# Performance work log

Measured on AMD Instinct MI355X. Metric: run time of the kernel, lower is better.

## Reference

```python
import jax, jax.numpy as jnp
import numpy as np

B, S, E, H = 4, 1024, 256, 12  # batch, seq, emb_dim, num_heads; per-head dim == E (module quirk)


def setup_inputs() -> dict:
    key = jax.random.key(0)
    ks = jax.random.split(key, 9)
    s = 0.02
    x = jax.random.normal(ks[0], (B, S, E), dtype=jnp.float32)
    # additive causal mask (the module's tril buffer is unused; mask arrives via attention_mask)
    causal = jnp.tril(jnp.ones((S, S), dtype=jnp.float32))
    attention_mask = ((1.0 - causal) * -10000.0)[None, None, :, :]
    Wq = jax.random.normal(ks[1], (E, E * H), dtype=jnp.float32) * s
    bq = jnp.zeros((E * H,), dtype=jnp.float32)
    Wk = jax.random.normal(ks[2], (E, E * H), dtype=jnp.float32) * s
    bk = jnp.zeros((E * H,), dtype=jnp.float32)
    Wv = jax.random.normal(ks[3], (E, E * H), dtype=jnp.float32) * s
    bv = jnp.zeros((E * H,), dtype=jnp.float32)
    Wfc = jax.random.normal(ks[4], (E * H, E), dtype=jnp.float32) * s
    bfc = jnp.zeros((E,), dtype=jnp.float32)
    return {"x": x, "attention_mask": attention_mask, "Wq": Wq, "bq": bq,
            "Wk": Wk, "bk": bk, "Wv": Wv, "bv": bv, "Wfc": Wfc, "bfc": bfc}


def _split_heads(t):
    # (B, S, H*E) -> (B, H, S, E)
    b, s, _ = t.shape
    return t.reshape(b, s, H, E).transpose(0, 2, 1, 3)


def reference(x, attention_mask, Wq, bq, Wk, bk, Wv, bv, Wfc, bfc):
    q = _split_heads(x @ Wq + bq)
    k = _split_heads(x @ Wk + bk)
    v = _split_heads(x @ Wv + bv)
    scale = 1.0 / jnp.sqrt(jnp.asarray(E, dtype=x.dtype))
    scores = jnp.einsum('bhqd,bhkd->bhqk', q, k) * scale + attention_mask
    probs = jax.nn.softmax(scores, axis=-1)  # dropout p=0 in eval reference
    ctx = jnp.einsum('bhqk,bhkd->bhqd', probs, v)
    merged = ctx.transpose(0, 2, 1, 3).reshape(x.shape[0], x.shape[1], H * E)
    return merged @ Wfc + bfc
```

## Files before the change

kernel.cpp:

```cpp
#include <hip/hip_runtime.h>

#define BATCH 4
#define SEQ   1024
#define EMB   256
#define NH    12
#define EH    3072
#define MROWS 4096

typedef __attribute__((ext_vector_type(8))) short bf16x8;
typedef __attribute__((ext_vector_type(4))) float f32x4;
typedef __attribute__((ext_vector_type(4))) short short4v;

__device__ __forceinline__ short f2bf(float f) {
  union { float f; unsigned u; } x; x.f = f;
  unsigned r = x.u + 0x7fffu + ((x.u >> 16) & 1u);
  return (short)(r >> 16);
}

__device__ __forceinline__ unsigned pack_trunc(float a, float b) {
  union { float f; unsigned u; } x, y;
  x.f = a; y.f = b;
  return (x.u >> 16) | (y.u & 0xffff0000u);
}

__device__ __forceinline__ void gload_lds16(const void* g, void* l) {
  __builtin_amdgcn_global_load_lds(
      (const __attribute__((address_space(1))) unsigned*)g,
      (__attribute__((address_space(3))) unsigned*)l, 16, 0, 0);
}

__global__ __launch_bounds__(256) void cast_x_kernel(const float* __restrict__ in,
                                                     short* __restrict__ out) {
  int i = (blockIdx.x * 256 + threadIdx.x) * 4;
  float4 v = *(const float4*)(in + i);
  short4v o;
  o[0] = f2bf(v.x); o[1] = f2bf(v.y); o[2] = f2bf(v.z); o[3] = f2bf(v.w);
  *(short4v*)(out + i) = o;
}

__global__ __launch_bounds__(256) void transpose_qkv_kernel(const float* __restrict__ Wq,
                                                            const float* __restrict__ Wk,
                                                            const float* __restrict__ Wv,
                                                            short* __restrict__ Wt) {
  __shared__ float tile[32][33];
  const float* W = blockIdx.z == 0 ? Wq : (blockIdx.z == 1 ? Wk : Wv);
  short* o = Wt + (size_t)blockIdx.z * EH * EMB;
  const int n0 = blockIdx.x * 32, k0 = blockIdx.y * 32;
  const int tx = threadIdx.x & 31, ty = threadIdx.x >> 5;
#pragma unroll
  for (int i = 0; i < 4; i++)
    tile[ty + 8 * i][tx] = W[(size_t)(k0 + ty + 8 * i) * EH + n0 + tx];
  __syncthreads();
#pragma unroll
  for (int i = 0; i < 4; i++) {
    int nr = ty + 8 * i;
    o[(size_t)(n0 + nr) * EMB + k0 + tx] = f2bf(tile[tx][nr]);
  }
}

__global__ __launch_bounds__(256) void transpose_cast_kernel(const float* __restrict__ W,
                                                             short* __restrict__ Wt,
                                                             int K, int N) {
  __shared__ float tile[32][33];
  const int n0 = blockIdx.x * 32, k0 = blockIdx.y * 32;
  const int tx = threadIdx.x & 31, ty = threadIdx.x >> 5;
#pragma unroll
  for (int i = 0; i < 4; i++)
    tile[ty + 8 * i][tx] = W[(size_t)(k0 + ty + 8 * i) * N + n0 + tx];
  __syncthreads();
#pragma unroll
  for (int i = 0; i < 4; i++) {
    int nr = ty + 8 * i;
    Wt[(size_t)(n0 + nr) * K + k0 + tx] = f2bf(tile[tx][nr]);
  }
}

__global__ __launch_bounds__(256) void qkv_gemm_kernel(const short* __restrict__ A,
                                                       const short* __restrict__ Bt,
                                                       const float* __restrict__ bq,
                                                       const float* __restrict__ bk,
                                                       const float* __restrict__ bv,
                                                       short* __restrict__ qout,
                                                       short* __restrict__ kout,
                                                       short* __restrict__ vout) {
  constexpr int BM = 128, BK = 64, K = EMB;
  __shared__ short As[2][BM * BK];
  __shared__ short Bs[2][BM * BK];
  const int tid = threadIdx.x;
  const int w = tid >> 6, lane = tid & 63;
  const int wm = w >> 1, wn = w & 1;
  const int l15 = lane & 15, l4 = lane >> 4;
  const int m0 = blockIdx.x * BM, n0 = blockIdx.y * BM;

  f32x4 acc[4][4] = {};

  int srow[4], scol[4];
#pragma unroll
  for (int i = 0; i < 4; i++) {
    const int idx = i * 256 + tid;
    const int row = idx >> 3, sp = idx & 7, sl = sp ^ (row & 7);
    srow[i] = row;
    scol[i] = sl * 8;
  }

#define QKV_STAGE(bu, k0)                                                        \
  {                                                                              \
    _Pragma("unroll") for (int i = 0; i < 4; i++) {                              \
      const int idx = i * 256 + tid;                                             \
      gload_lds16(A + (size_t)(m0 + srow[i]) * K + (k0) + scol[i],               \
                  (char*)&As[bu][0] + idx * 16);                                 \
      gload_lds16(Bt + (size_t)(n0 + srow[i]) * K + (k0) + scol[i],              \
                  (char*)&Bs[bu][0] + idx * 16);                                 \
    }                                                                            \
  }

  QKV_STAGE(0, 0);
  asm volatile("s_waitcnt vmcnt(0)" ::: "memory");
  __syncthreads();

  int bu = 0;
  for (int k0 = 0; k0 < K; k0 += BK) {
    if (k0 + BK < K) QKV_STAGE(bu ^ 1, k0 + BK);

#pragma unroll
    for (int kst = 0; kst < 2; kst++) {
      const int sp = (kst * 4 + l4) ^ (l15 & 7);
      bf16x8 af[4], bfr[4];
#pragma unroll
      for (int mt = 0; mt < 4; mt++)
        af[mt] = *(const bf16x8*)&As[bu][(wm * 64 + mt * 16 + l15) * 64 + sp * 8];
#pragma unroll
      for (int nt = 0; nt < 4; nt++)
        bfr[nt] = *(const bf16x8*)&Bs[bu][(wn * 64 + nt * 16 + l15) * 64 + sp * 8];
      __builtin_amdgcn_s_setprio(1);
#pragma unroll
      for (int mt = 0; mt < 4; mt++)
#pragma unroll
        for (int nt = 0; nt < 4; nt++)
          acc[mt][nt] = __builtin_amdgcn_mfma_f32_16x16x32_bf16(af[mt], bfr[nt], acc[mt][nt], 0, 0, 0);
      __builtin_amdgcn_s_setprio(0);
    }

    asm volatile("s_waitcnt vmcnt(0)" ::: "memory");
    __syncthreads();
    bu ^= 1;
  }

  const int region = n0 / 3072;
  const float* bias = region == 0 ? bq : (region == 1 ? bk : bv);
  const float kQScale = 0.09016844f;
#pragma unroll
  for (int nt = 0; nt < 4; nt++) {
    const int n = n0 + wn * 64 + nt * 16 + l15;
    const int col = n - region * 3072;
    const float bvv = bias[col];
#pragma unroll
    for (int mt = 0; mt < 4; mt++) {
      const int mrow = m0 + wm * 64 + mt * 16 + 4 * l4;
      f32x4 v = acc[mt][nt];
      if (region == 0) {
#pragma unroll
        for (int r = 0; r < 4; r++)
          qout[(size_t)(mrow + r) * EH + col] = f2bf((v[r] + bvv) * kQScale);
      } else if (region == 1) {
#pragma unroll
        for (int r = 0; r < 4; r++)
          kout[(size_t)(mrow + r) * EH + col] = f2bf(v[r] + bvv);
      } else {
        const int bb = mrow >> 10;
        const int s  = mrow & 1023;
        const int h  = col >> 8, d = col & 255;
        short4v o4;
        o4[0] = f2bf(v[0] + bvv); o4[1] = f2bf(v[1] + bvv);
        o4[2] = f2bf(v[2] + bvv); o4[3] = f2bf(v[3] + bvv);
        *(short4v*)&vout[((size_t)(bb * NH + h) * EMB + d) * SEQ + s] = o4;
      }
    }
  }
#undef QKV_STAGE
}

__global__ __launch_bounds__(256) void fc_partial_kernel(const short* __restrict__ A,
                                                         const short* __restrict__ Bt,
                                                         float* __restrict__ Pout,
                                                         int M, int N, int K) {
  constexpr int BM = 64, BK = 128, KSL = 768;
  __shared__ short As[2][BM * BK];
  __shared__ short Bs[2][BM * BK];
  const int tid = threadIdx.x;
  const int w = tid >> 6, lane = tid & 63;
  const int wm = w >> 1, wn = w & 1;
  const int l15 = lane & 15, l4 = lane >> 4;
  const int m0 = blockIdx.x * BM, n0 = blockIdx.y * BM;
  const int kbase = blockIdx.z * KSL;
  float* P = Pout + (size_t)blockIdx.z * M * N;

  f32x4 acc[2][2] = {};

  int srow[4], scol[4];
#pragma unroll
  for (int i = 0; i < 4; i++) {
    const int idx = i * 256 + tid;
    const int row = idx >> 4, sp = idx & 15, sl = sp ^ (row & 15);
    srow[i] = row;
    scol[i] = sl * 8;
  }

#define FC_STAGE(bu, k0)                                                         \
  {                                                                              \
    _Pragma("unroll") for (int i = 0; i < 4; i++) {                              \
      const int idx = i * 256 + tid;                                             \
      gload_lds16(A + (size_t)(m0 + srow[i]) * K + (k0) + scol[i],               \
                  (char*)&As[bu][0] + idx * 16);                                 \
      gload_lds16(Bt + (size_t)(n0 + srow[i]) * K + (k0) + scol[i],              \
                  (char*)&Bs[bu][0] + idx * 16);                                 \
    }                                                                            \
  }

  FC_STAGE(0, kbase);
  asm volatile("s_waitcnt vmcnt(0)" ::: "memory");
  __syncthreads();

  int bu = 0;
  for (int k0 = kbase; k0 < kbase + KSL; k0 += BK) {
    if (k0 + BK < kbase + KSL) FC_STAGE(bu ^ 1, k0 + BK);

#pragma unroll
    for (int kst = 0; kst < 4; kst++) {
      const int sp = (kst * 4 + l4) ^ l15;
      bf16x8 af[2], bfr[2];
#pragma unroll
      for (int mt = 0; mt < 2; mt++)
        af[mt] = *(const bf16x8*)&As[bu][(wm * 32 + mt * 16 + l15) * 128 + sp * 8];
#pragma unroll
      for (int nt = 0; nt < 2; nt++)
        bfr[nt] = *(const bf16x8*)&Bs[bu][(wn * 32 + nt * 16 + l15) * 128 + sp * 8];
      __builtin_amdgcn_s_setprio(1);
#pragma unroll
      for (int mt = 0; mt < 2; mt++)
#pragma unroll
        for (int nt = 0; nt < 2; nt++)
          acc[mt][nt] = __builtin_amdgcn_mfma_f32_16x16x32_bf16(af[mt], bfr[nt], acc[mt][nt], 0, 0, 0);
      __builtin_amdgcn_s_setprio(0);
    }

    asm volatile("s_waitcnt vmcnt(0)" ::: "memory");
    __syncthreads();
    bu ^= 1;
  }

#pragma unroll
  for (int nt = 0; nt < 2; nt++) {
    const int n = n0 + wn * 32 + nt * 16 + l15;
#pragma unroll
    for (int mt = 0; mt < 2; mt++) {
      const int mrow = m0 + wm * 32 + mt * 16 + 4 * l4;
      f32x4 v = acc[mt][nt];
#pragma unroll
      for (int r = 0; r < 4; r++)
        P[(size_t)(mrow + r) * N + n] = v[r];
    }
  }
#undef FC_STAGE
}

__global__ __launch_bounds__(256) void fc_reduce_kernel(const float* __restrict__ Pin,
                                                        const float* __restrict__ bias,
                                                        float* __restrict__ out) {
  const int i4 = (blockIdx.x * 256 + threadIdx.x) * 4;
  const int n = i4 & 255;
  float4 s = *(const float4*)(bias + n);
#pragma unroll
  for (int ks = 0; ks < 4; ks++) {
    float4 p = *(const float4*)(Pin + (size_t)ks * MROWS * EMB + i4);
    s.x += p.x; s.y += p.y; s.z += p.z; s.w += p.w;
  }
  *(float4*)(out + i4) = s;
}

__global__ __launch_bounds__(512) void attn_kernel(const short* __restrict__ Q,
                                                   const short* __restrict__ Kg,
                                                   const short* __restrict__ Vt,
                                                   short* __restrict__ Ctx) {
  __shared__ short Ks[2][8192];
  __shared__ short Vs[2][8192];
  __shared__ short Ps[8][512];
  const int tid = threadIdx.x, w = tid >> 6, lane = tid & 63;
  const int l15 = lane & 15, l4 = lane >> 4;
  const int bh = blockIdx.x, b = bh / NH, h = bh % NH;
  const int slot = blockIdx.y;

  const float kMaskL2 = -14426.95f;
  const float kThrL2  = 11.5f;

  const short* Kbase = Kg + (size_t)b * SEQ * EH + h * EMB;
  const short* Vbase = Vt + (size_t)bh * EMB * SEQ;

  int koff[2], voff[2];
#pragma unroll
  for (int i = 0; i < 2; i++) {
    const int idx = i * 512 + tid;
    {
      const int kv = (idx >> 3) & 31, sp = idx & 7, sl = sp ^ (kv & 7);
      koff[i] = kv * EH + (idx >> 8) * 64 + sl * 8;
    }
    {
      const int dp = idx >> 3, sp = idx & 7, sl = sp ^ (dp & 7);
      voff[i] = (dp * 2 + (sl >> 2)) * SEQ + (sl & 3) * 8;
    }
  }

  for (int pass = 0; pass < 2; pass++) {
    const int qt = (pass == 0) ? (7 - slot) : (slot - 2);
    if (qt < 0) continue;
    const int q0 = qt * 128;
    const int qw0 = q0 + w * 16;
    const int ntiles = 4 * qt + 4;

    bf16x8 qf[8];
    {
      const short* qp = Q + (size_t)(b * SEQ + qw0 + l15) * EH + h * EMB + 8 * l4;
#pragma unroll
      for (int kst = 0; kst < 8; kst++) qf[kst] = *(const bf16x8*)(qp + 32 * kst);
    }

#pragma unroll
    for (int i = 0; i < 2; i++) {
      const int idx = i * 512 + tid;
      gload_lds16(Kbase + koff[i], (char*)&Ks[0][0] + idx * 16);
      gload_lds16(Vbase + voff[i], (char*)&Vs[0][0] + idx * 16);
    }
    asm volatile("s_waitcnt vmcnt(0)" ::: "memory");
    __syncthreads();

    f32x4 o[16] = {};
    float mst = -1e30f, lst = 0.f;

    int bu = 0;
    for (int t = 0; t < ntiles; t++) {
      const int kv0 = t * 32;

      if (t + 1 < ntiles) {
        const short* kp = Kbase + (size_t)(kv0 + 32) * EH;
        const short* vp = Vbase + kv0 + 32;
#pragma unroll
        for (int i = 0; i < 2; i++) {
          const int idx = i * 512 + tid;
          gload_lds16(kp + koff[i], (char*)&Ks[bu ^ 1][0] + idx * 16);
          gload_lds16(vp + voff[i], (char*)&Vs[bu ^ 1][0] + idx * 16);
        }
      }

      if (kv0 <= qw0 + 15) {
        f32x4 sf[2] = {};
        __builtin_amdgcn_s_setprio(1);
#pragma unroll
        for (int nt = 0; nt < 2; nt++)
#pragma unroll
          for (int kst = 0; kst < 8; kst++) {
            const int sp = (((kst & 1) << 2) + l4) ^ (l15 & 7);
            bf16x8 kf = *(const bf16x8*)&Ks[bu][(kst >> 1) * 2048 + (nt * 16 + l15) * 64 + sp * 8];
            sf[nt] = __builtin_amdgcn_mfma_f32_16x16x32_bf16(kf, qf[kst], sf[nt], 0, 0, 0);
          }
        __builtin_amdgcn_s_setprio(0);

        const bool maskt = (kv0 + 31 > qw0);
        float sval[2][4];
        float mxl = -1e30f;
#pragma unroll
        for (int nt = 0; nt < 2; nt++)
#pragma unroll
          for (int r = 0; r < 4; r++) {
            float s = sf[nt][r];
            if (maskt) {
              const int kv = kv0 + nt * 16 + 4 * l4 + r;
              s += (kv > qw0 + l15) ? kMaskL2 : 0.0f;
            }
            sval[nt][r] = s;
            mxl = fmaxf(mxl, s);
          }
        float mx = fmaxf(mxl, __shfl_xor(mxl, 16));
        mx = fmaxf(mx, __shfl_xor(mx, 32));
        const bool skipt = __all(mx <= mst + kThrL2);
        float mref, fsc;
        if (skipt) {
          fsc = 1.0f;
          mref = mst;
        } else {
          float mnew = fmaxf(mst, mx);
          fsc = exp2f(mst - mnew);
          mst = mnew;
          mref = mnew;
        }
        float pp[2][4];
        float lsum = 0.f;
#pragma unroll
        for (int nt = 0; nt < 2; nt++)
#pragma unroll
          for (int r = 0; r < 4; r++) {
            float e = exp2f(sval[nt][r] - mref);
            pp[nt][r] = e;
            lsum += e;
          }
        lst = lst * fsc + lsum;

        if (!skipt) {
          float fv[4];
#pragma unroll
          for (int r = 0; r < 4; r++)
            fv[r] = __shfl(fsc, (lane & 48) + 4 * (lane >> 4) + r);
#pragma unroll
          for (int nt = 0; nt < 16; nt++) {
            o[nt][0] *= fv[0]; o[nt][1] *= fv[1];
            o[nt][2] *= fv[2]; o[nt][3] *= fv[3];
          }
        }

#pragma unroll
        for (int nt = 0; nt < 2; nt++) {
          uint2 pk;
          pk.x = pack_trunc(pp[nt][0], pp[nt][1]);
          pk.y = pack_trunc(pp[nt][2], pp[nt][3]);
          const int col0 = nt * 16 + 4 * l4;
          const int pseg = (col0 >> 3) ^ ((l15 >> 1) & 3);
          *(uint2*)&Ps[w][l15 * 32 + pseg * 8 + (col0 & 7)] = pk;
        }

        const int aseg = l4 ^ ((l15 >> 1) & 3);
        bf16x8 af = *(const bf16x8*)&Ps[w][l15 * 32 + aseg * 8];
        const int vsp = ((l15 & 1) * 4 + l4) ^ (l15 >> 1);
        __builtin_amdgcn_s_setprio(1);
#pragma unroll
        for (int nt = 0; nt < 16; nt++) {
          const int dp = nt * 8 + (l15 >> 1);
          bf16x8 vf = *(const bf16x8*)&Vs[bu][dp * 64 + vsp * 8];
          o[nt] = __builtin_amdgcn_mfma_f32_16x16x32_bf16(af, vf, o[nt], 0, 0, 0);
        }
        __builtin_amdgcn_s_setprio(0);
      }

      asm volatile("s_waitcnt vmcnt(0)" ::: "memory");
      __syncthreads();
      bu ^= 1;
    }

    lst += __shfl_xor(lst, 16);
    lst += __shfl_xor(lst, 32);
    const float inv = 1.f / lst;
    float invv[4];
#pragma unroll
    for (int r = 0; r < 4; r++)
      invv[r] = __shfl(inv, (lane & 48) + 4 * (lane >> 4) + r);

    const int mrow = b * SEQ + qw0 + 4 * l4;
#pragma unroll
    for (int nt = 0; nt < 16; nt++) {
      const int d = h * EMB + nt * 16 + l15;
#pragma unroll
      for (int r = 0; r < 4; r++)
        Ctx[(size_t)(mrow + r) * EH + d] = f2bf(o[nt][r] * invv[r]);
    }
  }
}

extern "C" void kernel_launch(void* const* d_in, const int* in_sizes, int n_in,
                              void* d_out, int out_size, void* d_ws, size_t ws_size,
                              hipStream_t stream) {
  const float* x   = (const float*)d_in[0];
  const float* Wq  = (const float*)d_in[2];
  const float* bq  = (const float*)d_in[3];
  const float* Wk  = (const float*)d_in[4];
  const float* bk  = (const float*)d_in[5];
  const float* Wv  = (const float*)d_in[6];
  const float* bv  = (const float*)d_in[7];
  const float* Wfc = (const float*)d_in[8];
  const float* bfc = (const float*)d_in[9];
  float* out = (float*)d_out;

  short* ws    = (short*)d_ws;
  short* xb    = ws;
  short* wqkvt = xb + 1048576;
  short* wfct  = wqkvt + 3 * 786432;
  short* q     = wfct + 786432;
  short* k     = q + 12582912;
  short* vt    = k + 12582912;
  short* ctx   = vt + 12582912;
  float* fcp   = (float*)q;

  cast_x_kernel<<<1024, 256, 0, stream>>>(x, xb);
  transpose_qkv_kernel<<<dim3(EH / 32, EMB / 32, 3), 256, 0, stream>>>(Wq, Wk, Wv, wqkvt);
  transpose_cast_kernel<<<dim3(EMB / 32, EH / 32), 256, 0, stream>>>(Wfc, wfct, EH, EMB);

  qkv_gemm_kernel<<<dim3(MROWS / 128, 9216 / 128), 256, 0, stream>>>(
      xb, wqkvt, bq, bk, bv, q, k, vt);

  attn_kernel<<<dim3(BATCH * NH, 5), 512, 0, stream>>>(q, k, vt, ctx);

  fc_partial_kernel<<<dim3(MROWS / 64, EMB / 64, 4), 256, 0, stream>>>(
      ctx, wfct, fcp, MROWS, EMB, EH);
  fc_reduce_kernel<<<(MROWS * EMB / 4) / 256, 256, 0, stream>>>(fcp, bfc, out);
}
```

Before: 145.0 us.

## Double attention KV tile to 64 keys and vectorize Q/K epilogue stores

The attention kernel now processes 64 keys per iteration instead of 32, using two 32-key sub-buffers for K, V and P. This halves the number of barriers, prefetch issues and softmax rescale steps per query tile, and splits the QK dot product into two independent accumulator chains to add instruction-level parallelism. The QKV GEMM swaps the MFMA operand order for the Q/K regions so each lane holds 4 consecutive columns, which allows vectorized short4 stores and a float4 bias load. In exchange, LDS use doubles (Ks/Vs go from 64 KB to 128 KB total), which may lower occupancy, and causal masking now skips work only at the coarser 64-key granularity.

```diff
diff --git a/kernel.cpp b/kernel.cpp
--- a/kernel.cpp
+++ b/kernel.cpp
@@ -91,6 +91,8 @@
   const int wm = w >> 1, wn = w & 1;
   const int l15 = lane & 15, l4 = lane >> 4;
   const int m0 = blockIdx.x * BM, n0 = blockIdx.y * BM;
+  const int region = n0 / 3072;
+  const bool qk = (region < 2);
 
   f32x4 acc[4][4] = {};
 
@@ -133,11 +135,19 @@
       for (int nt = 0; nt < 4; nt++)
         bfr[nt] = *(const bf16x8*)&Bs[bu][(wn * 64 + nt * 16 + l15) * 64 + sp * 8];
       __builtin_amdgcn_s_setprio(1);
-#pragma unroll
-      for (int mt = 0; mt < 4; mt++)
-#pragma unroll
-        for (int nt = 0; nt < 4; nt++)
-          acc[mt][nt] = __builtin_amdgcn_mfma_f32_16x16x32_bf16(af[mt], bfr[nt], acc[mt][nt], 0, 0, 0);
+      if (qk) {
+#pragma unroll
+        for (int mt = 0; mt < 4; mt++)
+#pragma unroll
+          for (int nt = 0; nt < 4; nt++)
+            acc[mt][nt] = __builtin_amdgcn_mfma_f32_16x16x32_bf16(bfr[nt], af[mt], acc[mt][nt], 0, 0, 0);
+      } else {
+#pragma unroll
+        for (int mt = 0; mt < 4; mt++)
+#pragma unroll
+          for (int nt = 0; nt < 4; nt++)
+            acc[mt][nt] = __builtin_amdgcn_mfma_f32_16x16x32_bf16(af[mt], bfr[nt], acc[mt][nt], 0, 0, 0);
+      }
       __builtin_amdgcn_s_setprio(0);
     }
 
@@ -146,27 +156,37 @@
     bu ^= 1;
   }
 
-  const int region = n0 / 3072;
-  const float* bias = region == 0 ? bq : (region == 1 ? bk : bv);
   const float kQScale = 0.09016844f;
-#pragma unroll
-  for (int nt = 0; nt < 4; nt++) {
-    const int n = n0 + wn * 64 + nt * 16 + l15;
-    const int col = n - region * 3072;
-    const float bvv = bias[col];
-#pragma unroll
-    for (int mt = 0; mt < 4; mt++) {
-      const int mrow = m0 + wm * 64 + mt * 16 + 4 * l4;
-      f32x4 v = acc[mt][nt];
-      if (region == 0) {
-#pragma unroll
-        for (int r = 0; r < 4; r++)
-          qout[(size_t)(mrow + r) * EH + col] = f2bf((v[r] + bvv) * kQScale);
-      } else if (region == 1) {
-#pragma unroll
-        for (int r = 0; r < 4; r++)
-          kout[(size_t)(mrow + r) * EH + col] = f2bf(v[r] + bvv);
-      } else {
+  if (qk) {
+    short* C = region == 0 ? qout : kout;
+    const float* bias = region == 0 ? bq : bk;
+    const float sc = region == 0 ? kQScale : 1.0f;
+#pragma unroll
+    for (int nt = 0; nt < 4; nt++) {
+      const int coln0 = (n0 - region * 3072) + wn * 64 + nt * 16 + 4 * l4;
+      const float4 bv4 = *(const float4*)&bias[coln0];
+#pragma unroll
+      for (int mt = 0; mt < 4; mt++) {
+        const int m = m0 + wm * 64 + mt * 16 + l15;
+        f32x4 v = acc[mt][nt];
+        short4v o4;
+        o4[0] = f2bf((v[0] + bv4.x) * sc);
+        o4[1] = f2bf((v[1] + bv4.y) * sc);
+        o4[2] = f2bf((v[2] + bv4.z) * sc);
+        o4[3] = f2bf((v[3] + bv4.w) * sc);
+        *(short4v*)&C[(size_t)m * EH + coln0] = o4;
+      }
+    }
+  } else {
+#pragma unroll
+    for (int nt = 0; nt < 4; nt++) {
+      const int n = n0 + wn * 64 + nt * 16 + l15;
+      const int col = n - 2 * 3072;
+      const float bvv = bv[col];
+#pragma unroll
+      for (int mt = 0; mt < 4; mt++) {
+        const int mrow = m0 + wm * 64 + mt * 16 + 4 * l4;
+        f32x4 v = acc[mt][nt];
         const int bb = mrow >> 10;
         const int s  = mrow & 1023;
         const int h  = col >> 8, d = col & 255;
@@ -282,9 +302,9 @@
                                                    const short* __restrict__ Kg,
                                                    const short* __restrict__ Vt,
                                                    short* __restrict__ Ctx) {
-  __shared__ short Ks[2][8192];
-  __shared__ short Vs[2][8192];
-  __shared__ short Ps[8][512];
+  __shared__ short Ks[2][2][8192];
+  __shared__ short Vs[2][2][8192];
+  __shared__ short Ps[8][2][512];
   const int tid = threadIdx.x, w = tid >> 6, lane = tid & 63;
   const int l15 = lane & 15, l4 = lane >> 4;
   const int bh = blockIdx.x, b = bh / NH, h = bh % NH;
@@ -296,17 +316,18 @@
   const short* Kbase = Kg + (size_t)b * SEQ * EH + h * EMB;
   const short* Vbase = Vt + (size_t)bh * EMB * SEQ;
 
-  int koff[2], voff[2];
-#pragma unroll
-  for (int i = 0; i < 2; i++) {
+  int koff[4], voff[4];
+#pragma unroll
+  for (int i = 0; i < 4; i++) {
     const int idx = i * 512 + tid;
+    const int hh = idx >> 10, ix = idx & 1023;
     {
-      const int kv = (idx >> 3) & 31, sp = idx & 7, sl = sp ^ (kv & 7);
-      koff[i] = kv * EH + (idx >> 8) * 64 + sl * 8;
+      const int kv = (ix >> 3) & 31, sp = ix & 7, sl = sp ^ (kv & 7);
+      koff[i] = (hh * 32 + kv) * EH + (ix >> 8) * 64 + sl * 8;
     }
     {
-      const int dp = idx >> 3, sp = idx & 7, sl = sp ^ (dp & 7);
-      voff[i] = (dp * 2 + (sl >> 2)) * SEQ + (sl & 3) * 8;
+      const int dp = ix >> 3, sp = ix & 7, sl = sp ^ (dp & 7);
+      voff[i] = (dp * 2 + (sl >> 2)) * SEQ + hh * 32 + (sl & 3) * 8;
     }
   }
 
@@ -315,7 +336,7 @@
     if (qt < 0) continue;
     const int q0 = qt * 128;
     const int qw0 = q0 + w * 16;
-    const int ntiles = 4 * qt + 4;
+    const int ntiles = 2 * qt + 2;
 
     bf16x8 qf[8];
     {
@@ -325,10 +346,10 @@
     }
 
 #pragma unroll
-    for (int i = 0; i < 2; i++) {
+    for (int i = 0; i < 4; i++) {
       const int idx = i * 512 + tid;
-      gload_lds16(Kbase + koff[i], (char*)&Ks[0][0] + idx * 16);
-      gload_lds16(Vbase + voff[i], (char*)&Vs[0][0] + idx * 16);
+      gload_lds16(Kbase + koff[i], (char*)&Ks[0][0][0] + idx * 16);
+      gload_lds16(Vbase + voff[i], (char*)&Vs[0][0][0] + idx * 16);
     }
     asm volatile("s_waitcnt vmcnt(0)" ::: "memory");
     __syncthreads();
@@ -338,40 +359,49 @@
 
     int bu = 0;
     for (int t = 0; t < ntiles; t++) {
-      const int kv0 = t * 32;
+      const int kv0 = t * 64;
 
       if (t + 1 < ntiles) {
-        const short* kp = Kbase + (size_t)(kv0 + 32) * EH;
-        const short* vp = Vbase + kv0 + 32;
-#pragma unroll
-        for (int i = 0; i < 2; i++) {
+        const short* kp = Kbase + (size_t)(kv0 + 64) * EH;
+        const short* vp = Vbase + kv0 + 64;
+#pragma unroll
+        for (int i = 0; i < 4; i++) {
           const int idx = i * 512 + tid;
-          gload_lds16(kp + koff[i], (char*)&Ks[bu ^ 1][0] + idx * 16);
-          gload_lds16(vp + voff[i], (char*)&Vs[bu ^ 1][0] + idx * 16);
+          gload_lds16(kp + koff[i], (char*)&Ks[bu ^ 1][0][0] + idx * 16);
+          gload_lds16(vp + voff[i], (char*)&Vs[bu ^ 1][0][0] + idx * 16);
         }
       }
 
       if (kv0 <= qw0 + 15) {
-        f32x4 sf[2] = {};
+        f32x4 sfa[4] = {}, sfb[4] = {};
         __builtin_amdgcn_s_setprio(1);
 #pragma unroll
-        for (int nt = 0; nt < 2; nt++)
-#pragma unroll
-          for (int kst = 0; kst < 8; kst++) {
+        for (int nt = 0; nt < 4; nt++) {
+          const short* ksh = &Ks[bu][nt >> 1][0];
+          const int rowoff = ((nt & 1) * 16 + l15) * 64;
+#pragma unroll
+          for (int kst = 0; kst < 4; kst++) {
             const int sp = (((kst & 1) << 2) + l4) ^ (l15 & 7);
-            bf16x8 kf = *(const bf16x8*)&Ks[bu][(kst >> 1) * 2048 + (nt * 16 + l15) * 64 + sp * 8];
-            sf[nt] = __builtin_amdgcn_mfma_f32_16x16x32_bf16(kf, qf[kst], sf[nt], 0, 0, 0);
+            bf16x8 kf = *(const bf16x8*)&ksh[(kst >> 1) * 2048 + rowoff + sp * 8];
+            sfa[nt] = __builtin_amdgcn_mfma_f32_16x16x32_bf16(kf, qf[kst], sfa[nt], 0, 0, 0);
           }
+#pragma unroll
+          for (int kst = 4; kst < 8; kst++) {
+            const int sp = (((kst & 1) << 2) + l4) ^ (l15 & 7);
+            bf16x8 kf = *(const bf16x8*)&ksh[(kst >> 1) * 2048 + rowoff + sp * 8];
+            sfb[nt] = __builtin_amdgcn_mfma_f32_16x16x32_bf16(kf, qf[kst], sfb[nt], 0, 0, 0);
+          }
+        }
         __builtin_amdgcn_s_setprio(0);
 
-        const bool maskt = (kv0 + 31 > qw0);
-        float sval[2][4];
+        const bool maskt = (kv0 + 63 > qw0);
+        float sval[4][4];
         float mxl = -1e30f;
 #pragma unroll
-        for (int nt = 0; nt < 2; nt++)
+        for (int nt = 0; nt < 4; nt++)
 #pragma unroll
           for (int r = 0; r < 4; r++) {
-            float s = sf[nt][r];
+            float s = sfa[nt][r] + sfb[nt][r];
             if (maskt) {
               const int kv = kv0 + nt * 16 + 4 * l4 + r;
               s += (kv > qw0 + l15) ? kMaskL2 : 0.0f;
@@ -392,10 +422,10 @@
           mst = mnew;
           mref = mnew;
         }
-        float pp[2][4];
+        float pp[4][4];
         float lsum = 0.f;
 #pragma unroll
-        for (int nt = 0; nt < 2; nt++)
+        for (int nt = 0; nt < 4; nt++)
 #pragma unroll
           for (int r = 0; r < 4; r++) {
             float e = exp2f(sval[nt][r] - mref);
@@ -417,24 +447,27 @@
         }
 
 #pragma unroll
-        for (int nt = 0; nt < 2; nt++) {
+        for (int nt = 0; nt < 4; nt++) {
           uint2 pk;
           pk.x = pack_trunc(pp[nt][0], pp[nt][1]);
           pk.y = pack_trunc(pp[nt][2], pp[nt][3]);
-          const int col0 = nt * 16 + 4 * l4;
+          const int col0 = (nt & 1) * 16 + 4 * l4;
           const int pseg = (col0 >> 3) ^ ((l15 >> 1) & 3);
-          *(uint2*)&Ps[w][l15 * 32 + pseg * 8 + (col0 & 7)] = pk;
+          *(uint2*)&Ps[w][nt >> 1][l15 * 32 + pseg * 8 + (col0 & 7)] = pk;
         }
 
         const int aseg = l4 ^ ((l15 >> 1) & 3);
-        bf16x8 af = *(const bf16x8*)&Ps[w][l15 * 32 + aseg * 8];
+        bf16x8 af0 = *(const bf16x8*)&Ps[w][0][l15 * 32 + aseg * 8];
+        bf16x8 af1 = *(const bf16x8*)&Ps[w][1][l15 * 32 + aseg * 8];
         const int vsp = ((l15 & 1) * 4 + l4) ^ (l15 >> 1);
         __builtin_amdgcn_s_setprio(1);
 #pragma unroll
         for (int nt = 0; nt < 16; nt++) {
           const int dp = nt * 8 + (l15 >> 1);
-          bf16x8 vf = *(const bf16x8*)&Vs[bu][dp * 64 + vsp * 8];
-          o[nt] = __builtin_amdgcn_mfma_f32_16x16x32_bf16(af, vf, o[nt], 0, 0, 0);
+          bf16x8 vf0 = *(const bf16x8*)&Vs[bu][0][dp * 64 + vsp * 8];
+          bf16x8 vf1 = *(const bf16x8*)&Vs[bu][1][dp * 64 + vsp * 8];
+          o[nt] = __builtin_amdgcn_mfma_f32_16x16x32_bf16(af0, vf0, o[nt], 0, 0, 0);
+          o[nt] = __builtin_amdgcn_mfma_f32_16x16x32_bf16(af1, vf1, o[nt], 0, 0, 0);
         }
         __builtin_amdgcn_s_setprio(0);
       }
```

Measured after the change: 135.4 us. -6.6%, faster.
